# Performance work log

Measured on AMD Instinct MI355X. Metric: run time of the kernel, lower is better.

The kernel has to match this reference:

```python
import jax, jax.numpy as jnp
import numpy as np

B, S, E, H = 2, 4096, 768, 12
D = E // H  # head_dim = 64
SCALE = D ** -0.5
NEG = -1e9


def setup_inputs() -> dict:
    key = jax.random.key(0)
    ks = jax.random.split(key, 10)
    init = lambda k, shape: jax.random.normal(k, shape, dtype=jnp.float32) * (shape[-1] ** -0.5)
    x = jax.random.normal(ks[0], (B, S, E), dtype=jnp.float32)
    attention_mask = jnp.zeros((B, 1, S, S), dtype=jnp.float32)
    # additive causal mask: 0 on/below diagonal, -1e9 above
    causal = jnp.where(jnp.tril(jnp.ones((S, S), dtype=bool)), 0.0, NEG).astype(jnp.float32)
    causal_attention_mask = causal[None, None]
    return {
        "x": x,
        "attention_mask": attention_mask,
        "causal_attention_mask": causal_attention_mask,
        "Wq": init(ks[1], (E, E)), "bq": jnp.zeros((E,), jnp.float32),
        "Wk": init(ks[2], (E, E)), "bk": jnp.zeros((E,), jnp.float32),
        "Wv": init(ks[3], (E, E)), "bv": jnp.zeros((E,), jnp.float32),
        "Wo": init(ks[4], (E, E)), "bo": jnp.zeros((E,), jnp.float32),
    }


def _split_heads(t):
    # [B,S,E] -> [B,H,S,D]
    return t.reshape(B, S, H, D).transpose(0, 2, 1, 3)


def reference(x, attention_mask, causal_attention_mask, Wq, bq, Wk, bk, Wv, bv, Wo, bo):
    q = _split_heads(x @ Wq.T + bq)
    k = _split_heads(x @ Wk.T + bk)
    v = _split_heads(x @ Wv.T + bv)
    mask = attention_mask + causal_attention_mask  # [B,1,S,S]
    scores = jnp.einsum("bhqd,bhkd->bhqk", q, k) * SCALE + mask
    probs = jax.nn.softmax(scores.astype(jnp.float32), axis=-1).astype(q.dtype)
    out = jnp.einsum("bhqk,bhkd->bhqd", probs, v)
    out = out.transpose(0, 2, 1, 3).reshape(B, S, E)
    return out @ Wo.T + bo
```

## Files before the change

kernel.cpp:

```cpp
#include <hip/hip_runtime.h>
#include <hip/hip_bf16.h>
#include <stdint.h>

#define B_ 2
#define S_ 4096
#define E_ 768
#define H_ 12
#define D_ 64
#define M_TOT (B_*S_)
#define NQKV (3*E_)

typedef __attribute__((ext_vector_type(8)))  short bf16x8;
typedef __attribute__((ext_vector_type(4)))  float f32x4;
typedef __attribute__((ext_vector_type(16))) float f32x16;
typedef unsigned short u16;
typedef unsigned int   u32;

__device__ __forceinline__ u16 f2bf(float f) {
  __hip_bfloat16 h = __float2bfloat16(f);
  return *reinterpret_cast<u16*>(&h);
}

__device__ __forceinline__ u32 cvtpk(float lo, float hi) {
  u32 r;
  asm("v_cvt_pk_bf16_f32 %0, %1, %2" : "=v"(r) : "v"(lo), "v"(hi));
  return r;
}

#define GLDS(gp, lp) __builtin_amdgcn_global_load_lds( \
    (const __attribute__((address_space(1))) void*)(gp), \
    (__attribute__((address_space(3))) void*)(lp), 16, 0, 0)


__global__ void k_cast_x(const float* __restrict__ x, u16* __restrict__ xb) {
  int i = blockIdx.x * blockDim.x + threadIdx.x;
  float4 v = reinterpret_cast<const float4*>(x)[i];
  ushort4 o;
  o.x = f2bf(v.x); o.y = f2bf(v.y); o.z = f2bf(v.z); o.w = f2bf(v.w);
  reinterpret_cast<ushort4*>(xb)[i] = o;
}

__global__ void k_pack_wqkv(const float* __restrict__ Wq, const float* __restrict__ Wk,
                            const float* __restrict__ Wv, const float* __restrict__ bq,
                            const float* __restrict__ bk, const float* __restrict__ bv,
                            u16* __restrict__ wqkv, float* __restrict__ bqkv) {
  int i = blockIdx.x * blockDim.x + threadIdx.x;
  int base = i * 4;
  int n = base / E_;
  int k = base % E_;
  const float* src; float sc;
  if (n < E_)        { src = Wq + (size_t)n*E_ + k;          sc = 0.125f; }
  else if (n < 2*E_) { src = Wk + (size_t)(n-E_)*E_ + k;     sc = 1.f; }
  else               { src = Wv + (size_t)(n-2*E_)*E_ + k;   sc = 1.f; }
  float4 v = *reinterpret_cast<const float4*>(src);
  ushort4 o;
  o.x = f2bf(v.x*sc); o.y = f2bf(v.y*sc); o.z = f2bf(v.z*sc); o.w = f2bf(v.w*sc);
  reinterpret_cast<ushort4*>(wqkv)[i] = o;
  if (i < NQKV) {
    float b = (i < E_) ? bq[i]*0.125f : (i < 2*E_) ? bk[i-E_] : bv[i-2*E_];
    bqkv[i] = b;
  }
}

__global__ void k_cast_wo(const float* __restrict__ Wo, u16* __restrict__ wo) {
  int i = blockIdx.x * blockDim.x + threadIdx.x;
  float4 v = reinterpret_cast<const float4*>(Wo)[i];
  ushort4 o;
  o.x = f2bf(v.x); o.y = f2bf(v.y); o.z = f2bf(v.z); o.w = f2bf(v.w);
  reinterpret_cast<ushort4*>(wo)[i] = o;
}


template<int MODE>
__global__ __launch_bounds__(256)
void k_gemm(const u16* __restrict__ A, const u16* __restrict__ W,
            const float* __restrict__ bias,
            u16* __restrict__ dq, u16* __restrict__ dk, u16* __restrict__ dv,
            float* __restrict__ fout)
{
  __shared__ u16 As[128*64];
  __shared__ u16 Ws[128*64];
  const int tid  = threadIdx.x;
  const int lane = tid & 63, wave = tid >> 6;
  const int m0 = blockIdx.x * 128;
  const int n0 = blockIdx.y * 128;
  const int g  = lane >> 4, cc = lane & 15;
  const int wr = (wave >> 1) * 64, wc = (wave & 1) * 64;
  const int srow = lane >> 3;
  const int scol = (lane & 7) * 8;

  f32x4 acc[4][4];
  #pragma unroll
  for (int m = 0; m < 4; ++m)
    #pragma unroll
    for (int n = 0; n < 4; ++n) acc[m][n] = (f32x4){0.f,0.f,0.f,0.f};

  for (int k0 = 0; k0 < E_; k0 += 64) {
    __syncthreads();
    #pragma unroll
    for (int i = 0; i < 4; ++i) {
      const int r0 = (i*4 + wave) * 8;
      GLDS(A + (size_t)(m0 + r0 + srow)*E_ + k0 + scol, As + r0*64);
      GLDS(W + (size_t)(n0 + r0 + srow)*E_ + k0 + scol, Ws + r0*64);
    }
    __syncthreads();
    #pragma unroll
    for (int kk = 0; kk < 64; kk += 32) {
      bf16x8 af[4], bfr[4];
      #pragma unroll
      for (int m = 0; m < 4; ++m)
        af[m] = *reinterpret_cast<const bf16x8*>(As + (wr + m*16 + cc)*64 + kk + g*8);
      #pragma unroll
      for (int n = 0; n < 4; ++n)
        bfr[n] = *reinterpret_cast<const bf16x8*>(Ws + (wc + n*16 + cc)*64 + kk + g*8);
      #pragma unroll
      for (int m = 0; m < 4; ++m)
        #pragma unroll
        for (int n = 0; n < 4; ++n)
          acc[m][n] = __builtin_amdgcn_mfma_f32_16x16x32_bf16(af[m], bfr[n], acc[m][n], 0, 0, 0);
    }
  }

  #pragma unroll
  for (int n = 0; n < 4; ++n) {
    const int colg = n0 + wc + n*16 + cc;
    const float bb = bias[colg];
    if (MODE == 0) {
      const int which = colg / E_;
      const int nn = colg % E_;
      const int h = nn >> 6, d = nn & 63;
      #pragma unroll
      for (int m = 0; m < 4; ++m)
        #pragma unroll
        for (int j = 0; j < 4; ++j) {
          const int row = m0 + wr + m*16 + g*4 + j;
          const int b = row >> 12, s = row & (S_-1);
          const u16 val = f2bf(acc[m][n][j] + bb);
          if (which == 0)       dq[(((size_t)b*H_ + h)*S_ + s)*D_ + d] = val;
          else if (which == 1)  dk[(((size_t)b*H_ + h)*S_ + s)*D_ + d] = val;
          else                  dv[(((size_t)b*H_ + h)*D_ + d)*S_ + s] = val;
        }
    } else {
      #pragma unroll
      for (int m = 0; m < 4; ++m)
        #pragma unroll
        for (int j = 0; j < 4; ++j) {
          const int row = m0 + wr + m*16 + g*4 + j;
          fout[(size_t)row*E_ + colg] = acc[m][n][j] + bb;
        }
    }
  }
}


__global__ __launch_bounds__(256, 3)
void k_attn(const u16* __restrict__ Qb, const u16* __restrict__ Kb,
            const u16* __restrict__ Vtg, u16* __restrict__ AO)
{
  __shared__ u16 Ks[2][32*128];
  __shared__ u16 Vs[2][32*128];
  const int tid = threadIdx.x, lane = tid & 63, w = tid >> 6;

  const int L = blockIdx.x;
  const int xcd = L & 7, kk_ = L >> 3;
  const int bh = xcd * 3 + (kk_ >> 5);
  const int qt = 31 - (kk_ & 31);
  const int q0 = qt * 128;
  const int ntiles = 2*qt + 2;

  const size_t kbase = (size_t)bh * S_ * D_;
  const size_t vbase = (size_t)bh * D_ * S_;
  const int hi = lane >> 5, l31 = lane & 31;
  const int swz = (lane & 15) << 4;
  const int qg = q0 + w*32 + l31;

  int stA[2], stB[2];
  #pragma unroll
  for (int i = 0; i < 2; ++i) {
    const int j = 2*w + i;
    const int row = j*4 + (lane >> 4);
    const int gb = ((lane & 15) * 16) ^ ((row & 15) << 4);
    stA[i] = row + 32*(gb >> 7);
    stB[i] = (gb & 127) >> 1;
  }

  bf16x8 qf[4];
  #pragma unroll
  for (int ds = 0; ds < 4; ++ds)
    qf[ds] = *reinterpret_cast<const bf16x8*>(Qb + kbase + (size_t)qg*D_ + ds*16 + hi*8);

  float m_run = -INFINITY, l_run = 0.f;
  f32x16 o0, o1;
  #pragma unroll
  for (int r = 0; r < 16; ++r) { o0[r] = 0.f; o1[r] = 0.f; }

#define STAGE(buf, kv0_) do { \
    _Pragma("unroll") \
    for (int i = 0; i < 2; ++i) { \
      GLDS(Kb  + kbase + (size_t)((kv0_) + stA[i])*D_ + stB[i], &Ks[buf][(2*w+i)*512]); \
      GLDS(Vtg + vbase + (size_t)stA[i]*S_ + (kv0_) + stB[i],   &Vs[buf][(2*w+i)*512]); \
    } } while(0)

  int cur = 0;
  STAGE(0, 0);

  for (int t = 0; t < ntiles; ++t) {
    const int kv0 = t * 64;
    asm volatile("s_waitcnt vmcnt(0)" ::: "memory");
    __builtin_amdgcn_s_barrier();
    asm volatile("" ::: "memory");
    if (t + 1 < ntiles) STAGE(cur ^ 1, (t+1)*64);

    const u16* bK = Ks[cur];
    const u16* bV = Vs[cur];

    f32x16 s0, s1;
    #pragma unroll
    for (int r = 0; r < 16; ++r) { s0[r] = 0.f; s1[r] = 0.f; }
    #pragma unroll
    for (int ds = 0; ds < 4; ++ds) {
      const int off = ((32*ds + 16*hi) ^ swz) >> 1;
      bf16x8 a0 = *reinterpret_cast<const bf16x8*>(bK + l31*128 + off);
      bf16x8 a1 = *reinterpret_cast<const bf16x8*>(bK + l31*128 + (off ^ 64));
      s0 = __builtin_amdgcn_mfma_f32_32x32x16_bf16(a0, qf[ds], s0, 0, 0, 0);
      s1 = __builtin_amdgcn_mfma_f32_32x32x16_bf16(a1, qf[ds], s1, 0, 0, 0);
    }

    if (t >= ntiles - 2) {
      #pragma unroll
      for (int r = 0; r < 16; ++r) {
        const int kvl = kv0 + (r&3) + 8*(r>>2) + 4*hi;
        s0[r] = (kvl      > qg) ? -1e30f : s0[r];
        s1[r] = (kvl + 32 > qg) ? -1e30f : s1[r];
      }
    }

    float mx = s0[0];
    #pragma unroll
    for (int r = 1; r < 16; ++r) mx = fmaxf(mx, s0[r]);
    #pragma unroll
    for (int r = 0; r < 16; ++r) mx = fmaxf(mx, s1[r]);
    mx = fmaxf(mx, __shfl_xor(mx, 32));
    const float mnew  = fmaxf(m_run, mx);
    const float alpha = __expf(m_run - mnew);
    m_run = mnew;
    float sum = 0.f;
    #pragma unroll
    for (int r = 0; r < 16; ++r) { s0[r] = __expf(s0[r] - mnew); sum += s0[r]; }
    #pragma unroll
    for (int r = 0; r < 16; ++r) { s1[r] = __expf(s1[r] - mnew); sum += s1[r]; }
    sum += __shfl_xor(sum, 32);
    l_run = l_run * alpha + sum;
    #pragma unroll
    for (int r = 0; r < 16; ++r) { o0[r] *= alpha; o1[r] *= alpha; }

    u32 c[16];
    #pragma unroll
    for (int i = 0; i < 8; ++i) {
      c[i]   = cvtpk(s0[2*i], s0[2*i+1]);
      c[8+i] = cvtpk(s1[2*i], s1[2*i+1]);
    }

    #pragma unroll
    for (int ks = 0; ks < 4; ++ks) {
      const int cb = (ks>>1)*8 + (ks&1)*4;
      u32 x0 = c[cb],   y0 = c[cb+2];
      u32 x1 = c[cb+1], y1 = c[cb+3];
      asm volatile("v_permlane32_swap_b32 %0, %1" : "+v"(x0), "+v"(y0));
      asm volatile("v_permlane32_swap_b32 %0, %1" : "+v"(x1), "+v"(y1));
      union { u32 u[4]; bf16x8 v; } pf;
      pf.u[0] = x0; pf.u[1] = x1; pf.u[2] = y0; pf.u[3] = y1;
      const int voff = ((32*ks + 16*hi) ^ swz) >> 1;
      bf16x8 v0 = *reinterpret_cast<const bf16x8*>(bV + l31*128 + voff);
      bf16x8 v1 = *reinterpret_cast<const bf16x8*>(bV + l31*128 + (voff ^ 64));
      o0 = __builtin_amdgcn_mfma_f32_32x32x16_bf16(v0, pf.v, o0, 0, 0, 0);
      o1 = __builtin_amdgcn_mfma_f32_32x32x16_bf16(v1, pf.v, o1, 0, 0, 0);
    }

    asm volatile("" ::: "memory");
    __builtin_amdgcn_s_barrier();
    cur ^= 1;
  }
#undef STAGE

  const int b = bh / H_, h = bh % H_;
  const float inv = 1.0f / l_run;
  u16* dst = AO + ((size_t)b*S_ + qg)*E_ + h*64;
  #pragma unroll
  for (int aa = 0; aa < 4; ++aa) {
    ushort4 wv;
    wv.x = f2bf(o0[4*aa+0]*inv); wv.y = f2bf(o0[4*aa+1]*inv);
    wv.z = f2bf(o0[4*aa+2]*inv); wv.w = f2bf(o0[4*aa+3]*inv);
    *reinterpret_cast<ushort4*>(dst + aa*8 + hi*4) = wv;
  }
  #pragma unroll
  for (int aa = 0; aa < 4; ++aa) {
    ushort4 wv;
    wv.x = f2bf(o1[4*aa+0]*inv); wv.y = f2bf(o1[4*aa+1]*inv);
    wv.z = f2bf(o1[4*aa+2]*inv); wv.w = f2bf(o1[4*aa+3]*inv);
    *reinterpret_cast<ushort4*>(dst + 32 + aa*8 + hi*4) = wv;
  }
}


extern "C" void kernel_launch(void* const* d_in, const int* in_sizes, int n_in,
                              void* d_out, int out_size, void* d_ws, size_t ws_size,
                              hipStream_t stream) {
  const float* x  = (const float*)d_in[0];
  const float* Wq = (const float*)d_in[3];
  const float* bq = (const float*)d_in[4];
  const float* Wk = (const float*)d_in[5];
  const float* bk = (const float*)d_in[6];
  const float* Wv = (const float*)d_in[7];
  const float* bv = (const float*)d_in[8];
  const float* Wo = (const float*)d_in[9];
  const float* bo = (const float*)d_in[10];
  float* out = (float*)d_out;

  const size_t SZ_X   = (size_t)M_TOT * E_ * 2;
  const size_t SZ_WQKV= (size_t)NQKV * E_ * 2;
  const size_t SZ_WO  = (size_t)E_ * E_ * 2;
  const size_t SZ_B   = (size_t)NQKV * 4;
  char* w = (char*)d_ws;
  u16*   xb   = (u16*)(w);
  u16*   wqkv = (u16*)(w + SZ_X);
  u16*   wob  = (u16*)(w + SZ_X + SZ_WQKV);
  float* bqkv = (float*)(w + SZ_X + SZ_WQKV + SZ_WO);
  char*  w2   = w + SZ_X + SZ_WQKV + SZ_WO + SZ_B;
  u16* Qb = (u16*)(w2);
  u16* Kb = (u16*)(w2 + SZ_X);
  u16* Vb = (u16*)(w2 + 2*SZ_X);
  u16* AO = (u16*)(w2 + 3*SZ_X);

  k_cast_x  <<<6144, 256, 0, stream>>>(x, xb);
  k_pack_wqkv<<<1728, 256, 0, stream>>>(Wq, Wk, Wv, bq, bk, bv, wqkv, bqkv);
  k_cast_wo <<<576,  256, 0, stream>>>(Wo, wob);

  dim3 gq(64, 18);
  k_gemm<0><<<gq, 256, 0, stream>>>(xb, wqkv, bqkv, Qb, Kb, Vb, nullptr);

  k_attn<<<768, 256, 0, stream>>>(Qb, Kb, Vb, AO);

  dim3 go(64, 6);
  k_gemm<1><<<go, 256, 0, stream>>>(AO, wob, bo, nullptr, nullptr, nullptr, out);
}
```

Measured before the change: 243.2 us.

## Split attention into 64-row q tiles, use exp2 with lazy rescale and setprio

Folds log2(e) into the Q scale so the softmax can use exp2f. Attention blocks shrink to 128 threads (two waves) covering 64 query rows, so the grid grows to 1536 blocks with a plain bh/qt mapping instead of the XCD-aware one. The online softmax now rescales the running output only when the tile max exceeds the running max by more than 8 (in log2 units), and its max and sum reductions are tree-shaped. MFMA sections are wrapped in s_setprio. Smaller blocks make each block load every K/V tile for fewer query rows, which roughly doubles K/V traffic, and dropping the XCD mapping may cost L2 locality.

```diff
diff --git a/kernel.cpp b/kernel.cpp
--- a/kernel.cpp
+++ b/kernel.cpp
@@ -39,6 +39,8 @@
   o.x = f2bf(v.x); o.y = f2bf(v.y); o.z = f2bf(v.z); o.w = f2bf(v.w);
   reinterpret_cast<ushort4*>(xb)[i] = o;
 }
+
+#define QSCALE 0.1803368801111573f
 
 __global__ void k_pack_wqkv(const float* __restrict__ Wq, const float* __restrict__ Wk,
                             const float* __restrict__ Wv, const float* __restrict__ bq,
@@ -49,7 +51,7 @@
   int n = base / E_;
   int k = base % E_;
   const float* src; float sc;
-  if (n < E_)        { src = Wq + (size_t)n*E_ + k;          sc = 0.125f; }
+  if (n < E_)        { src = Wq + (size_t)n*E_ + k;          sc = QSCALE; }
   else if (n < 2*E_) { src = Wk + (size_t)(n-E_)*E_ + k;     sc = 1.f; }
   else               { src = Wv + (size_t)(n-2*E_)*E_ + k;   sc = 1.f; }
   float4 v = *reinterpret_cast<const float4*>(src);
@@ -57,7 +59,7 @@
   o.x = f2bf(v.x*sc); o.y = f2bf(v.y*sc); o.z = f2bf(v.z*sc); o.w = f2bf(v.w*sc);
   reinterpret_cast<ushort4*>(wqkv)[i] = o;
   if (i < NQKV) {
-    float b = (i < E_) ? bq[i]*0.125f : (i < 2*E_) ? bk[i-E_] : bv[i-2*E_];
+    float b = (i < E_) ? bq[i]*QSCALE : (i < 2*E_) ? bk[i-E_] : bv[i-2*E_];
     bqkv[i] = b;
   }
 }
@@ -153,7 +155,7 @@
 }
 
 
-__global__ __launch_bounds__(256, 3)
+__global__ __launch_bounds__(128, 2)
 void k_attn(const u16* __restrict__ Qb, const u16* __restrict__ Kb,
             const u16* __restrict__ Vtg, u16* __restrict__ AO)
 {
@@ -162,11 +164,10 @@
   const int tid = threadIdx.x, lane = tid & 63, w = tid >> 6;
 
   const int L = blockIdx.x;
-  const int xcd = L & 7, kk_ = L >> 3;
-  const int bh = xcd * 3 + (kk_ >> 5);
-  const int qt = 31 - (kk_ & 31);
-  const int q0 = qt * 128;
-  const int ntiles = 2*qt + 2;
+  const int bh = L % 24;
+  const int qt = 63 - L / 24;
+  const int q0 = qt * 64;
+  const int ntiles = qt + 1;
 
   const size_t kbase = (size_t)bh * S_ * D_;
   const size_t vbase = (size_t)bh * D_ * S_;
@@ -174,10 +175,10 @@
   const int swz = (lane & 15) << 4;
   const int qg = q0 + w*32 + l31;
 
-  int stA[2], stB[2];
-  #pragma unroll
-  for (int i = 0; i < 2; ++i) {
-    const int j = 2*w + i;
+  int stA[4], stB[4];
+  #pragma unroll
+  for (int i = 0; i < 4; ++i) {
+    const int j = 4*w + i;
     const int row = j*4 + (lane >> 4);
     const int gb = ((lane & 15) * 16) ^ ((row & 15) << 4);
     stA[i] = row + 32*(gb >> 7);
@@ -196,9 +197,9 @@
 
 #define STAGE(buf, kv0_) do { \
     _Pragma("unroll") \
-    for (int i = 0; i < 2; ++i) { \
-      GLDS(Kb  + kbase + (size_t)((kv0_) + stA[i])*D_ + stB[i], &Ks[buf][(2*w+i)*512]); \
-      GLDS(Vtg + vbase + (size_t)stA[i]*S_ + (kv0_) + stB[i],   &Vs[buf][(2*w+i)*512]); \
+    for (int i = 0; i < 4; ++i) { \
+      GLDS(Kb  + kbase + (size_t)((kv0_) + stA[i])*D_ + stB[i], &Ks[buf][(4*w+i)*512]); \
+      GLDS(Vtg + vbase + (size_t)stA[i]*S_ + (kv0_) + stB[i],   &Vs[buf][(4*w+i)*512]); \
     } } while(0)
 
   int cur = 0;
@@ -217,6 +218,7 @@
     f32x16 s0, s1;
     #pragma unroll
     for (int r = 0; r < 16; ++r) { s0[r] = 0.f; s1[r] = 0.f; }
+    __builtin_amdgcn_s_setprio(1);
     #pragma unroll
     for (int ds = 0; ds < 4; ++ds) {
       const int off = ((32*ds + 16*hi) ^ swz) >> 1;
@@ -225,8 +227,9 @@
       s0 = __builtin_amdgcn_mfma_f32_32x32x16_bf16(a0, qf[ds], s0, 0, 0, 0);
       s1 = __builtin_amdgcn_mfma_f32_32x32x16_bf16(a1, qf[ds], s1, 0, 0, 0);
     }
-
-    if (t >= ntiles - 2) {
+    __builtin_amdgcn_s_setprio(0);
+
+    if (t == ntiles - 1) {
       #pragma unroll
       for (int r = 0; r < 16; ++r) {
         const int kvl = kv0 + (r&3) + 8*(r>>2) + 4*hi;
@@ -235,24 +238,40 @@
       }
     }
 
-    float mx = s0[0];
-    #pragma unroll
-    for (int r = 1; r < 16; ++r) mx = fmaxf(mx, s0[r]);
-    #pragma unroll
-    for (int r = 0; r < 16; ++r) mx = fmaxf(mx, s1[r]);
+    float m4[8];
+    #pragma unroll
+    for (int i = 0; i < 4; ++i)
+      m4[i] = fmaxf(fmaxf(s0[4*i], s0[4*i+1]), fmaxf(s0[4*i+2], s0[4*i+3]));
+    #pragma unroll
+    for (int i = 0; i < 4; ++i)
+      m4[4+i] = fmaxf(fmaxf(s1[4*i], s1[4*i+1]), fmaxf(s1[4*i+2], s1[4*i+3]));
+    float mx = fmaxf(fmaxf(fmaxf(m4[0], m4[1]), fmaxf(m4[2], m4[3])),
+                     fmaxf(fmaxf(m4[4], m4[5]), fmaxf(m4[6], m4[7])));
     mx = fmaxf(mx, __shfl_xor(mx, 32));
-    const float mnew  = fmaxf(m_run, mx);
-    const float alpha = __expf(m_run - mnew);
-    m_run = mnew;
-    float sum = 0.f;
-    #pragma unroll
-    for (int r = 0; r < 16; ++r) { s0[r] = __expf(s0[r] - mnew); sum += s0[r]; }
-    #pragma unroll
-    for (int r = 0; r < 16; ++r) { s1[r] = __expf(s1[r] - mnew); sum += s1[r]; }
+
+    if (!__all(mx <= m_run + 8.0f)) {
+      const float mnew  = fmaxf(m_run, mx);
+      const float alpha = exp2f(m_run - mnew);
+      m_run = mnew;
+      l_run *= alpha;
+      #pragma unroll
+      for (int r = 0; r < 16; ++r) { o0[r] *= alpha; o1[r] *= alpha; }
+    }
+
+    #pragma unroll
+    for (int r = 0; r < 16; ++r) s0[r] = exp2f(s0[r] - m_run);
+    #pragma unroll
+    for (int r = 0; r < 16; ++r) s1[r] = exp2f(s1[r] - m_run);
+    float t4[8];
+    #pragma unroll
+    for (int i = 0; i < 4; ++i)
+      t4[i] = (s0[4*i] + s0[4*i+1]) + (s0[4*i+2] + s0[4*i+3]);
+    #pragma unroll
+    for (int i = 0; i < 4; ++i)
+      t4[4+i] = (s1[4*i] + s1[4*i+1]) + (s1[4*i+2] + s1[4*i+3]);
+    float sum = ((t4[0]+t4[1]) + (t4[2]+t4[3])) + ((t4[4]+t4[5]) + (t4[6]+t4[7]));
     sum += __shfl_xor(sum, 32);
-    l_run = l_run * alpha + sum;
-    #pragma unroll
-    for (int r = 0; r < 16; ++r) { o0[r] *= alpha; o1[r] *= alpha; }
+    l_run += sum;
 
     u32 c[16];
     #pragma unroll
@@ -273,8 +292,10 @@
       const int voff = ((32*ks + 16*hi) ^ swz) >> 1;
       bf16x8 v0 = *reinterpret_cast<const bf16x8*>(bV + l31*128 + voff);
       bf16x8 v1 = *reinterpret_cast<const bf16x8*>(bV + l31*128 + (voff ^ 64));
+      __builtin_amdgcn_s_setprio(1);
       o0 = __builtin_amdgcn_mfma_f32_32x32x16_bf16(v0, pf.v, o0, 0, 0, 0);
       o1 = __builtin_amdgcn_mfma_f32_32x32x16_bf16(v1, pf.v, o1, 0, 0, 0);
+      __builtin_amdgcn_s_setprio(0);
     }
 
     asm volatile("" ::: "memory");
@@ -339,7 +360,7 @@
   dim3 gq(64, 18);
   k_gemm<0><<<gq, 256, 0, stream>>>(xb, wqkv, bqkv, Qb, Kb, Vb, nullptr);
 
-  k_attn<<<768, 256, 0, stream>>>(Qb, Kb, Vb, AO);
+  k_attn<<<1536, 128, 0, stream>>>(Qb, Kb, Vb, AO);
 
   dim3 go(64, 6);
   k_gemm<1><<<go, 256, 0, stream>>>(AO, wob, bo, nullptr, nullptr, nullptr, out);
```

New measurement: 250.0 us. 2.8% more time.
